# Performance work log

Measured on AMD Instinct MI355X. Metric: run time of the kernel, lower is better.

The kernel has to match this reference:

```python
import jax, jax.numpy as jnp
import numpy as np
import math

HIDDEN = 256
GUMBEL_EPS = 1e-20
MASK_EPS = 1e-8
TAU = 1.0


def _gumbel(u):
    return -jnp.log(-jnp.log(u + GUMBEL_EPS) + GUMBEL_EPS)


def setup_inputs() -> dict:
    key = jax.random.key(0)
    ks = jax.random.split(key, 16)
    B, N = 16, 128
    goal_dim, obs_dim, local_dim, num_skills = 64, 128, 64, 16
    h = HIDDEN

    def lin(k, out_d, in_d):
        kw, kb = jax.random.split(k)
        bound = 1.0 / math.sqrt(in_d)
        W = jax.random.uniform(kw, (out_d, in_d), minval=-bound, maxval=bound, dtype=jnp.float32)
        b = jax.random.uniform(kb, (out_d,), minval=-bound, maxval=bound, dtype=jnp.float32)
        return W, b

    Wq, bq = lin(ks[0], h, goal_dim)
    Wk, bk = lin(ks[1], h, obs_dim)
    Wv, bv = lin(ks[2], h, obs_dim)
    Wo, bo = lin(ks[3], h, h)
    Ws, bs = lin(ks[4], num_skills, local_dim + goal_dim + h)

    return {
        "goals": jax.random.normal(ks[5], (B, N, goal_dim), dtype=jnp.float32),
        "agents": jax.random.normal(ks[6], (B, N, obs_dim), dtype=jnp.float32),
        "agents_local": jax.random.normal(ks[7], (B, N, local_dim), dtype=jnp.float32),
        "u1": jax.random.uniform(ks[8], (B, N, N), dtype=jnp.float32),
        "u2": jax.random.uniform(ks[9], (B, N, N), dtype=jnp.float32),
        "Wq": Wq, "bq": bq, "Wk": Wk, "bk": bk, "Wv": Wv, "bv": bv,
        "Wo": Wo, "bo": bo, "Ws": Ws, "bs": bs,
    }


def reference(goals, agents, agents_local, u1, u2, Wq, bq, Wk, bk, Wv, bv, Wo, bo, Ws, bs):
    # Projections
    Q = jnp.einsum('bnd,hd->bnh', goals, Wq) + bq   # [B,N,h]
    K = jnp.einsum('bmd,hd->bmh', agents, Wk) + bk  # [B,N,h]
    V = jnp.einsum('bmd,hd->bmh', agents, Wv) + bv  # [B,N,h]

    scale = math.sqrt(HIDDEN) + 1e-12
    logits = jnp.einsum('bnh,bmh->bnm', Q, K) / scale  # [B,N,N]

    # Gumbel-sigmoid mask (soft, hard=False)
    g1, g2 = _gumbel(u1), _gumbel(u2)
    mask = jax.nn.sigmoid((logits + g1 - g2) / TAU)  # [B,N,N]

    scores = logits + jnp.log(mask + MASK_EPS)
    attn = jax.nn.softmax(scores, axis=-1)  # [B,N,N]

    # info[b,n,h] = sum_m attn[b,n,m] * mask[b,n,m] * V[b,m,h]
    # (equivalent to (attn.unsqueeze(-1) * V_masked).sum(dim=2) without
    #  materializing the [B,N,N,h] V_masked tensor)
    info = jnp.einsum('bnm,bnm,bmh->bnh', attn, mask, V)

    out = jnp.einsum('bnh,gh->bng', info, Wo) + bo  # [B,N,h]

    concat = jnp.concatenate([agents_local, goals, out], axis=-1)
    logit = jnp.einsum('bnc,sc->bns', concat, Ws) + bs  # [B,N,num_skills]

    return (logit, mask, attn, out)
```

## Files before the change

### kernel.cpp

```cpp
#include <hip/hip_runtime.h>
#include <math.h>


typedef float f32x4 __attribute__((ext_vector_type(4)));
typedef short s16x8 __attribute__((ext_vector_type(8)));

#define WOBF_OFF  0
#define QBF_OFF   32768
#define KBF_OFF   294912
#define VTBF_OFF  557056

#define LOGIT_OFF 0
#define MASK_OFF  32768
#define ATTN_OFF  294912
#define OUT_OFF   557056

static __device__ __forceinline__ unsigned short f2bf(float x) {
  unsigned int u = __float_as_uint(x);
  u = (u + 0x7fffu + ((u >> 16) & 1u)) >> 16;
  return (unsigned short)u;
}
static __device__ __forceinline__ float bf2f(unsigned short h) {
  return __uint_as_float(((unsigned int)h) << 16);
}

static __device__ __forceinline__ void split8(const float* __restrict__ p,
                                              s16x8* hi, s16x8* lo) {
  float4 x0 = *(const float4*)p;
  float4 x1 = *(const float4*)(p + 4);
  float xs[8] = {x0.x, x0.y, x0.z, x0.w, x1.x, x1.y, x1.z, x1.w};
#pragma unroll
  for (int j = 0; j < 8; j++) {
    unsigned short h = f2bf(xs[j]);
    (*hi)[j] = (short)h;
    (*lo)[j] = (short)f2bf(xs[j] - bf2f(h));
  }
}
#define MFMA(a, b, c) __builtin_amdgcn_mfma_f32_16x16x32_bf16((a), (b), (c), 0, 0, 0)

__global__ __launch_bounds__(512) void proj_k(
    const float* __restrict__ goals, const float* __restrict__ agents,
    const float* __restrict__ Wq, const float* __restrict__ bq,
    const float* __restrict__ Wk, const float* __restrict__ bk,
    const float* __restrict__ Wv, const float* __restrict__ bv,
    const float* __restrict__ Wo, float* __restrict__ ws) {
  unsigned short* qbf  = (unsigned short*)(ws + QBF_OFF);
  unsigned short* kbf  = (unsigned short*)(ws + KBF_OFF);
  unsigned short* vtbf = (unsigned short*)(ws + VTBF_OFF);
  unsigned short* wobf = (unsigned short*)(ws + WOBF_OFF);

  __shared__ __align__(16) float xg[16 * 68];
  __shared__ __align__(16) float xa[16 * 132];

  int t = threadIdx.x;
  int bid = blockIdx.x;
  int xcd = bid & 7, j = bid >> 3;
  int bb = 2 * xcd + (j & 1);
  int sub = j >> 1;
  int r0 = bb * 128 + (sub >> 1) * 16;
  int colbase = (sub & 1) * 128;

  for (int i = t; i < 1024; i += 512) xg[(i >> 6) * 68 + (i & 63)] = goals[(size_t)r0 * 64 + i];
  for (int i = t; i < 2048; i += 512) xa[(i >> 7) * 132 + (i & 127)] = agents[(size_t)r0 * 128 + i];
  if (t < 256) {
    int jj = bid * 256 + t;
    wobf[jj] = f2bf(Wo[jj]);
  }
  __syncthreads();

  int w = t >> 6, l = t & 63, lr = l & 15, lc = l >> 4;
  int oc = colbase + w * 16 + lr;

  {
    f32x4 acc = {0.f, 0.f, 0.f, 0.f};
#pragma unroll
    for (int kk = 0; kk < 2; kk++) {
      s16x8 ahi, alo, bhi, blo;
      split8(&xg[lr * 68 + kk * 32 + lc * 8], &ahi, &alo);
      split8(&Wq[(size_t)oc * 64 + kk * 32 + lc * 8], &bhi, &blo);
      acc = MFMA(ahi, bhi, acc);
      acc = MFMA(alo, bhi, acc);
      acc = MFMA(ahi, blo, acc);
    }
    float bqv = bq[oc];
#pragma unroll
    for (int q = 0; q < 4; q++)
      qbf[(size_t)(r0 + 4 * lc + q) * 256 + oc] = f2bf(acc[q] + bqv);
  }
  {
    f32x4 acc = {0.f, 0.f, 0.f, 0.f};
#pragma unroll
    for (int kk = 0; kk < 4; kk++) {
      s16x8 ahi, alo, bhi, blo;
      split8(&xa[lr * 132 + kk * 32 + lc * 8], &ahi, &alo);
      split8(&Wk[(size_t)oc * 128 + kk * 32 + lc * 8], &bhi, &blo);
      acc = MFMA(ahi, bhi, acc);
      acc = MFMA(alo, bhi, acc);
      acc = MFMA(ahi, blo, acc);
    }
    float bkv = bk[oc];
#pragma unroll
    for (int q = 0; q < 4; q++)
      kbf[(size_t)(r0 + 4 * lc + q) * 256 + oc] = f2bf(acc[q] + bkv);
  }
  {
    f32x4 acc = {0.f, 0.f, 0.f, 0.f};
#pragma unroll
    for (int kk = 0; kk < 4; kk++) {
      s16x8 ahi, alo, bhi, blo;
      split8(&xa[lr * 132 + kk * 32 + lc * 8], &ahi, &alo);
      split8(&Wv[(size_t)oc * 128 + kk * 32 + lc * 8], &bhi, &blo);
      acc = MFMA(ahi, bhi, acc);
      acc = MFMA(alo, bhi, acc);
      acc = MFMA(ahi, blo, acc);
    }
    float bvv = bv[oc];
    int m0 = r0 & 127;
#pragma unroll
    for (int q = 0; q < 4; q++)
      vtbf[(size_t)(bb * 256 + oc) * 128 + m0 + 4 * lc + q] = f2bf(acc[q] + bvv);
  }
}

__global__ __launch_bounds__(1024) void attn_k(
    const float* __restrict__ goals, const float* __restrict__ agents_local,
    const float* __restrict__ u1, const float* __restrict__ u2,
    const float* __restrict__ bo, const float* __restrict__ Wsm,
    const float* __restrict__ bs, const float* __restrict__ ws,
    float* __restrict__ out) {
  const unsigned short* Qbf  = (const unsigned short*)(ws + QBF_OFF);
  const unsigned short* Kbf  = (const unsigned short*)(ws + KBF_OFF);
  const unsigned short* VTbf = (const unsigned short*)(ws + VTBF_OFF);
  const unsigned short* Wobf = (const unsigned short*)(ws + WOBF_OFF);
  float* o_logit = out + LOGIT_OFF;
  float* o_mask  = out + MASK_OFF;
  float* o_attn  = out + ATTN_OFF;
  float* o_out   = out + OUT_OFF;

  int bid = blockIdx.x;
  int xcd = bid & 7, idx = bid >> 3;
  int b  = 2 * xcd + (idx & 1);
  int n0 = (idx >> 1) << 3;
  int rtile = n0 & 0x70;
  int soff  = n0 & 8;
  int t = threadIdx.x;
  int w = t >> 6, l = t & 63, lr = l & 15, lc = l >> 4;

  __shared__ __align__(16) float Spp[2][8][132];
  __shared__ __align__(16) unsigned short Wb[16 * 136];
  __shared__ __align__(16) unsigned short Ib[16 * 264];
  __shared__ __align__(16) float outb[8 * 260];
  __shared__ float redmax[8][2], redsum[8][2];

  int pm = t & 127, prl = t >> 7;
  int prow = b * 128 + n0 + prl;
  float uu1 = __builtin_nontemporal_load(&u1[(size_t)prow * 128 + pm]);
  float uu2 = __builtin_nontemporal_load(&u2[(size_t)prow * 128 + pm]);
  int h0g = w * 16;
  float bov = bo[h0g + lr];
  const s16x8* vtp = (const s16x8*)(VTbf + (size_t)(b * 256 + h0g + lr) * 128);
  s16x8 fv0 = vtp[lc], fv1 = vtp[4 + lc], fv2 = vtp[8 + lc], fv3 = vtp[12 + lc];

  {
    int mt = w & 7, kh = w >> 3;
    const s16x8* ap = (const s16x8*)(Qbf + (size_t)(b * 128 + rtile + lr) * 256 + kh * 128);
    const s16x8* bp = (const s16x8*)(Kbf + (size_t)(b * 128 + mt * 16 + lr) * 256 + kh * 128);
    f32x4 acc = {0.f, 0.f, 0.f, 0.f};
#pragma unroll
    for (int kk = 0; kk < 4; kk++)
      acc = MFMA(ap[kk * 4 + lc], bp[kk * 4 + lc], acc);
    if ((lc >> 1) == (soff >> 3)) {
#pragma unroll
      for (int q = 0; q < 4; q++) Spp[kh][(4 * lc + q) & 7][mt * 16 + lr] = acc[q];
    }
    if (t < 544) ((unsigned int*)(Wb + (soff ^ 8) * 136))[t] = 0u;
  }
  __syncthreads();

  {
    int half = (t >> 6) & 1;
    float lg = (Spp[0][prl][pm] + Spp[1][prl][pm]) * 0.0625f;
    float g1 = -__logf(-__logf(uu1 + 1e-20f) + 1e-20f);
    float g2 = -__logf(-__logf(uu2 + 1e-20f) + 1e-20f);
    float mkv = 1.0f / (1.0f + __expf(-(lg + g1 - g2)));
    __builtin_nontemporal_store(mkv, &o_mask[(size_t)prow * 128 + pm]);
    float sc = lg + __logf(mkv + 1e-8f);
    float v = sc;
#pragma unroll
    for (int off = 32; off >= 1; off >>= 1) v = fmaxf(v, __shfl_xor(v, off));
    if (l == 0) redmax[prl][half] = v;
    __syncthreads();
    float rmax = fmaxf(redmax[prl][0], redmax[prl][1]);
    float e = __expf(sc - rmax);
    float s = e;
#pragma unroll
    for (int off = 32; off >= 1; off >>= 1) s += __shfl_xor(s, off);
    if (l == 0) redsum[prl][half] = s;
    __syncthreads();
    float rsum = redsum[prl][0] + redsum[prl][1];
    float attn = e / rsum;
    __builtin_nontemporal_store(attn, &o_attn[(size_t)prow * 128 + pm]);
    Wb[(soff + prl) * 136 + pm] = f2bf(attn * mkv);
  }
  __syncthreads();

  {
    s16x8 a0 = *(const s16x8*)(Wb + lr * 136 + 0 * 32 + lc * 8);
    s16x8 a1 = *(const s16x8*)(Wb + lr * 136 + 1 * 32 + lc * 8);
    s16x8 a2 = *(const s16x8*)(Wb + lr * 136 + 2 * 32 + lc * 8);
    s16x8 a3 = *(const s16x8*)(Wb + lr * 136 + 3 * 32 + lc * 8);
    f32x4 acc = {0.f, 0.f, 0.f, 0.f};
    acc = MFMA(a0, fv0, acc);
    acc = MFMA(a1, fv1, acc);
    acc = MFMA(a2, fv2, acc);
    acc = MFMA(a3, fv3, acc);
#pragma unroll
    for (int q = 0; q < 4; q++) Ib[(4 * lc + q) * 264 + h0g + lr] = f2bf(acc[q]);
  }
  __syncthreads();

  {
    int g0 = w * 16;
    f32x4 acc = {0.f, 0.f, 0.f, 0.f};
#pragma unroll
    for (int kk = 0; kk < 8; kk++) {
      s16x8 a = *(const s16x8*)(Ib + lr * 264 + kk * 32 + lc * 8);
      s16x8 bfr = *(const s16x8*)(Wobf + (size_t)(g0 + lr) * 256 + kk * 32 + lc * 8);
      acc = MFMA(a, bfr, acc);
    }
    if ((lc >> 1) == (soff >> 3)) {
#pragma unroll
      for (int q = 0; q < 4; q++) {
        int rloc = (4 * lc + q) & 7;
        float val = acc[q] + bov;
        __builtin_nontemporal_store(val, &o_out[(size_t)(b * 128 + n0 + rloc) * 256 + g0 + lr]);
        outb[rloc * 260 + g0 + lr] = val;
      }
    }
  }
  __syncthreads();

  {
    int rloc = t >> 7, s = (t >> 3) & 15, p = t & 7;
    int row = b * 128 + n0 + rloc;
    const float4* Ws4 = (const float4*)(Wsm + s * 384);
    const float4* lp4 = (const float4*)(agents_local + (size_t)row * 64);
    const float4* gp4 = (const float4*)(goals + (size_t)row * 64);
    float acc = 0.f;
#pragma unroll
    for (int i = 0; i < 12; i++) {
      int cc = p * 48 + i * 4;
      float4 c4;
      if (cc < 64)       c4 = lp4[cc >> 2];
      else if (cc < 128) c4 = gp4[(cc - 64) >> 2];
      else               c4 = *(const float4*)&outb[rloc * 260 + (cc - 128)];
      float4 w4 = Ws4[cc >> 2];
      acc = fmaf(w4.x, c4.x, fmaf(w4.y, c4.y, fmaf(w4.z, c4.z, fmaf(w4.w, c4.w, acc))));
    }
    acc += __shfl_xor(acc, 1);
    acc += __shfl_xor(acc, 2);
    acc += __shfl_xor(acc, 4);
    if (p == 0) __builtin_nontemporal_store(acc + bs[s], &o_logit[row * 16 + s]);
  }
}

extern "C" void kernel_launch(void* const* d_in, const int* in_sizes, int n_in,
                              void* d_out, int out_size, void* d_ws, size_t ws_size,
                              hipStream_t stream) {
  const float* goals        = (const float*)d_in[0];
  const float* agents       = (const float*)d_in[1];
  const float* agents_local = (const float*)d_in[2];
  const float* u1           = (const float*)d_in[3];
  const float* u2           = (const float*)d_in[4];
  const float* Wq = (const float*)d_in[5];
  const float* bq = (const float*)d_in[6];
  const float* Wk = (const float*)d_in[7];
  const float* bk = (const float*)d_in[8];
  const float* Wv = (const float*)d_in[9];
  const float* bv = (const float*)d_in[10];
  const float* Wo = (const float*)d_in[11];
  const float* bo = (const float*)d_in[12];
  const float* Wsm = (const float*)d_in[13];
  const float* bs  = (const float*)d_in[14];
  float* out = (float*)d_out;
  float* ws  = (float*)d_ws;

  proj_k<<<256, 512, 0, stream>>>(goals, agents, Wq, bq, Wk, bk, Wv, bv, Wo, ws);
  attn_k<<<256, 1024, 0, stream>>>(goals, agents_local, u1, u2, bo, Wsm, bs, ws, out);
}
```

Measured before the change: 33.83 us.

## Split attention kernel into 512 blocks of 4 rows with 512 threads

Reworks attn_k so each block handles 4 query rows instead of 8, launching 512 blocks of 512 threads instead of 256 blocks of 1024. The QK^T split-K over two halves is replaced by a full-K MFMA per wave. Each wave now covers two 16-column groups for the PV and Wo products. The aim is more blocks and better occupancy across CUs on a small problem. The cost is that Q/K/V^T/Wo fragments are reloaded by twice as many blocks and the MFMA tiles are mostly wasted on 4 useful rows out of 16.

```diff
diff --git a/kernel.cpp b/kernel.cpp
--- a/kernel.cpp
+++ b/kernel.cpp
@@ -122,7 +122,7 @@
   }
 }
 
-__global__ __launch_bounds__(1024) void attn_k(
+__global__ __launch_bounds__(512, 4) void attn_k(
     const float* __restrict__ goals, const float* __restrict__ agents_local,
     const float* __restrict__ u1, const float* __restrict__ u2,
     const float* __restrict__ bo, const float* __restrict__ Wsm,
@@ -140,46 +140,47 @@
   int bid = blockIdx.x;
   int xcd = bid & 7, idx = bid >> 3;
   int b  = 2 * xcd + (idx & 1);
-  int n0 = (idx >> 1) << 3;
+  int n0 = (idx >> 1) << 2;
   int rtile = n0 & 0x70;
-  int soff  = n0 & 8;
+  int soff  = n0 & 12;
   int t = threadIdx.x;
   int w = t >> 6, l = t & 63, lr = l & 15, lc = l >> 4;
 
-  __shared__ __align__(16) float Spp[2][8][132];
+  __shared__ __align__(16) float Sp[4][132];
   __shared__ __align__(16) unsigned short Wb[16 * 136];
   __shared__ __align__(16) unsigned short Ib[16 * 264];
-  __shared__ __align__(16) float outb[8 * 260];
-  __shared__ float redmax[8][2], redsum[8][2];
+  __shared__ __align__(16) float outb[4 * 260];
+  __shared__ float redmax[4][2], redsum[4][2];
 
   int pm = t & 127, prl = t >> 7;
   int prow = b * 128 + n0 + prl;
   float uu1 = __builtin_nontemporal_load(&u1[(size_t)prow * 128 + pm]);
   float uu2 = __builtin_nontemporal_load(&u2[(size_t)prow * 128 + pm]);
-  int h0g = w * 16;
-  float bov = bo[h0g + lr];
-  const s16x8* vtp = (const s16x8*)(VTbf + (size_t)(b * 256 + h0g + lr) * 128);
-  s16x8 fv0 = vtp[lc], fv1 = vtp[4 + lc], fv2 = vtp[8 + lc], fv3 = vtp[12 + lc];
-
-  {
-    int mt = w & 7, kh = w >> 3;
-    const s16x8* ap = (const s16x8*)(Qbf + (size_t)(b * 128 + rtile + lr) * 256 + kh * 128);
-    const s16x8* bp = (const s16x8*)(Kbf + (size_t)(b * 128 + mt * 16 + lr) * 256 + kh * 128);
+  float bov0 = bo[w * 16 + lr];
+  float bov1 = bo[(w + 8) * 16 + lr];
+  const s16x8* vtp0 = (const s16x8*)(VTbf + (size_t)(b * 256 + w * 16 + lr) * 128);
+  const s16x8* vtp1 = (const s16x8*)(VTbf + (size_t)(b * 256 + (w + 8) * 16 + lr) * 128);
+  s16x8 fv0 = vtp0[lc], fv1 = vtp0[4 + lc], fv2 = vtp0[8 + lc], fv3 = vtp0[12 + lc];
+  s16x8 fw0 = vtp1[lc], fw1 = vtp1[4 + lc], fw2 = vtp1[8 + lc], fw3 = vtp1[12 + lc];
+
+  {
+    const s16x8* ap = (const s16x8*)(Qbf + (size_t)(b * 128 + rtile + lr) * 256);
+    const s16x8* bp = (const s16x8*)(Kbf + (size_t)(b * 128 + w * 16 + lr) * 256);
     f32x4 acc = {0.f, 0.f, 0.f, 0.f};
 #pragma unroll
-    for (int kk = 0; kk < 4; kk++)
+    for (int kk = 0; kk < 8; kk++)
       acc = MFMA(ap[kk * 4 + lc], bp[kk * 4 + lc], acc);
-    if ((lc >> 1) == (soff >> 3)) {
-#pragma unroll
-      for (int q = 0; q < 4; q++) Spp[kh][(4 * lc + q) & 7][mt * 16 + lr] = acc[q];
-    }
-    if (t < 544) ((unsigned int*)(Wb + (soff ^ 8) * 136))[t] = 0u;
+    if (lc == (soff >> 2)) {
+#pragma unroll
+      for (int q = 0; q < 4; q++) Sp[q][w * 16 + lr] = acc[q] * 0.0625f;
+    }
+    for (int i = t; i < 1088; i += 512) ((unsigned int*)Wb)[i] = 0u;
   }
   __syncthreads();
 
   {
     int half = (t >> 6) & 1;
-    float lg = (Spp[0][prl][pm] + Spp[1][prl][pm]) * 0.0625f;
+    float lg = Sp[prl][pm];
     float g1 = -__logf(-__logf(uu1 + 1e-20f) + 1e-20f);
     float g2 = -__logf(-__logf(uu2 + 1e-20f) + 1e-20f);
     float mkv = 1.0f / (1.0f + __expf(-(lg + g1 - g2)));
@@ -209,32 +210,43 @@
     s16x8 a1 = *(const s16x8*)(Wb + lr * 136 + 1 * 32 + lc * 8);
     s16x8 a2 = *(const s16x8*)(Wb + lr * 136 + 2 * 32 + lc * 8);
     s16x8 a3 = *(const s16x8*)(Wb + lr * 136 + 3 * 32 + lc * 8);
-    f32x4 acc = {0.f, 0.f, 0.f, 0.f};
-    acc = MFMA(a0, fv0, acc);
-    acc = MFMA(a1, fv1, acc);
-    acc = MFMA(a2, fv2, acc);
-    acc = MFMA(a3, fv3, acc);
-#pragma unroll
-    for (int q = 0; q < 4; q++) Ib[(4 * lc + q) * 264 + h0g + lr] = f2bf(acc[q]);
-  }
-  __syncthreads();
-
-  {
-    int g0 = w * 16;
-    f32x4 acc = {0.f, 0.f, 0.f, 0.f};
-#pragma unroll
-    for (int kk = 0; kk < 8; kk++) {
-      s16x8 a = *(const s16x8*)(Ib + lr * 264 + kk * 32 + lc * 8);
-      s16x8 bfr = *(const s16x8*)(Wobf + (size_t)(g0 + lr) * 256 + kk * 32 + lc * 8);
-      acc = MFMA(a, bfr, acc);
-    }
-    if ((lc >> 1) == (soff >> 3)) {
-#pragma unroll
-      for (int q = 0; q < 4; q++) {
-        int rloc = (4 * lc + q) & 7;
-        float val = acc[q] + bov;
-        __builtin_nontemporal_store(val, &o_out[(size_t)(b * 128 + n0 + rloc) * 256 + g0 + lr]);
-        outb[rloc * 260 + g0 + lr] = val;
+    f32x4 acc0 = {0.f, 0.f, 0.f, 0.f};
+    acc0 = MFMA(a0, fv0, acc0);
+    acc0 = MFMA(a1, fv1, acc0);
+    acc0 = MFMA(a2, fv2, acc0);
+    acc0 = MFMA(a3, fv3, acc0);
+    f32x4 acc1 = {0.f, 0.f, 0.f, 0.f};
+    acc1 = MFMA(a0, fw0, acc1);
+    acc1 = MFMA(a1, fw1, acc1);
+    acc1 = MFMA(a2, fw2, acc1);
+    acc1 = MFMA(a3, fw3, acc1);
+#pragma unroll
+    for (int q = 0; q < 4; q++) {
+      Ib[(4 * lc + q) * 264 + w * 16 + lr] = f2bf(acc0[q]);
+      Ib[(4 * lc + q) * 264 + (w + 8) * 16 + lr] = f2bf(acc1[q]);
+    }
+  }
+  __syncthreads();
+
+  {
+#pragma unroll
+    for (int gs = 0; gs < 2; gs++) {
+      int g0 = (w + 8 * gs) * 16;
+      f32x4 acc = {0.f, 0.f, 0.f, 0.f};
+#pragma unroll
+      for (int kk = 0; kk < 8; kk++) {
+        s16x8 a = *(const s16x8*)(Ib + lr * 264 + kk * 32 + lc * 8);
+        s16x8 bfr = *(const s16x8*)(Wobf + (size_t)(g0 + lr) * 256 + kk * 32 + lc * 8);
+        acc = MFMA(a, bfr, acc);
+      }
+      float bov = gs ? bov1 : bov0;
+      if (lc == (soff >> 2)) {
+#pragma unroll
+        for (int q = 0; q < 4; q++) {
+          float val = acc[q] + bov;
+          __builtin_nontemporal_store(val, &o_out[(size_t)(b * 128 + n0 + q) * 256 + g0 + lr]);
+          outb[q * 260 + g0 + lr] = val;
+        }
       }
     }
   }
@@ -286,5 +298,5 @@
   float* ws  = (float*)d_ws;
 
   proj_k<<<256, 512, 0, stream>>>(goals, agents, Wq, bq, Wk, bk, Wv, bv, Wo, ws);
-  attn_k<<<256, 1024, 0, stream>>>(goals, agents_local, u1, u2, bo, Wsm, bs, ws, out);
-}
+  attn_k<<<512, 512, 0, stream>>>(goals, agents_local, u1, u2, bo, Wsm, bs, ws, out);
+}
```

Result: slower. 40.81 us (+20.6%).
